# Optimization experiments

Hardware: AMD Instinct MI355X
Metric: run time of the kernel (lower is better)

The kernel has to match this reference:

```python
import jax, jax.numpy as jnp
import numpy as np

B, S, D, H, DK, DFF = 4, 2048, 512, 8, 64, 2048
MAX_DIST = 2047  # effective_dist = min(MAX_DIST, S-1) = S-1, required by the skew reshape
EPS = 1e-6


def setup_inputs() -> dict:
    key = jax.random.key(0)
    ks = jax.random.split(key, 12)
    w = lambda k, shape: jax.random.normal(k, shape, jnp.float32) * 0.02
    return {
        "x": jax.random.normal(ks[0], (B, S, D), jnp.float32),
        "mask": jnp.tril(jnp.ones((1, 1, S, S), jnp.int32)),  # causal
        "wq": w(ks[1], (D, D)),
        "wk": w(ks[2], (D, D)),
        "wv": w(ks[3], (D, D)),
        "w0": w(ks[4], (D, D)),
        "b0": jnp.zeros((D,), jnp.float32),
        "rel_emb": w(ks[5], (H, MAX_DIST + 1, DK)),
        "ln1_g": jnp.ones((D,), jnp.float32),
        "ln1_b": jnp.zeros((D,), jnp.float32),
        "ln2_g": jnp.ones((D,), jnp.float32),
        "ln2_b": jnp.zeros((D,), jnp.float32),
        "ff_w1": w(ks[6], (D, DFF)),
        "ff_b1": jnp.zeros((DFF,), jnp.float32),
        "ff_w2": w(ks[7], (DFF, D)),
        "ff_b2": jnp.zeros((D,), jnp.float32),
    }


def _layernorm(t, g, b):
    mu = t.mean(-1, keepdims=True)
    var = ((t - mu) ** 2).mean(-1, keepdims=True)
    return (t - mu) * jax.lax.rsqrt(var + EPS) * g + b


def _rel_scores(q, rel_emb):
    # q: [B,H,S,DK]; rel_emb: [H, MAX_DIST+1, DK]
    eff = min(MAX_DIST, S - 1)                      # static
    q_er = jnp.einsum('bhid,hrd->bhir', q, rel_emb[:, :eff + 1])  # [B,H,S,S]
    padded = jnp.pad(q_er, ((0, 0), (0, 0), (0, 0), (1, 0)))      # [B,H,S,S+1]
    # skew trick: reinterpret and drop first row -> [B,H,S,S]
    return padded.reshape(B, H, S + 1, S)[:, :, 1:, :]


def reference(x, mask, wq, wk, wv, w0, b0, rel_emb,
              ln1_g, ln1_b, ln2_g, ln2_b, ff_w1, ff_b1, ff_w2, ff_b2):
    scale = float(np.sqrt(DK))
    # --- self-attention sublayer (pre-norm residual) ---
    h = _layernorm(x, ln1_g, ln1_b)
    q = (h @ wq).reshape(B, S, H, DK).transpose(0, 2, 1, 3)  # [B,H,S,DK]
    k = (h @ wk).reshape(B, S, H, DK).transpose(0, 2, 1, 3)
    v = (h @ wv).reshape(B, S, H, DK).transpose(0, 2, 1, 3)
    content = jnp.einsum('bhid,bhjd->bhij', q, k) / scale     # [B,H,S,S]
    scores = content + _rel_scores(q, rel_emb)
    scores = jnp.where(mask == 0, jnp.float32(-1e9), scores)
    probs = jax.nn.softmax(scores, axis=-1)
    attn = jnp.einsum('bhij,bhjd->bhid', probs, v)            # [B,H,S,DK]
    attn = attn.transpose(0, 2, 1, 3).reshape(B, S, D)
    x = x + (attn @ w0 + b0)
    # --- feed-forward sublayer (pre-norm residual) ---
    h2 = _layernorm(x, ln2_g, ln2_b)
    ff = jax.nn.relu(h2 @ ff_w1 + ff_b1) @ ff_w2 + ff_b2
    return x + ff
```

## Files before the change

kernel.cpp:

```cpp
#include <hip/hip_runtime.h>
#include <hip/hip_bf16.h>

#define SB 2048
#define DB 512
#define HB 8
#define DKB 64
#define DFB 2048
#define BATCH 4
#define BSTR 92

typedef __attribute__((ext_vector_type(8))) short bf16x8;
typedef __attribute__((ext_vector_type(4))) float f32x4;
typedef __attribute__((ext_vector_type(2))) float f32x2;
typedef __attribute__((ext_vector_type(2))) unsigned u32x2;
typedef __attribute__((ext_vector_type(4))) short s16x4;

static __device__ __forceinline__ short f2bf(float x) {
  union { float f; unsigned u; } v; v.f = x;
  unsigned r = (v.u + 0x7fffu + ((v.u >> 16) & 1u)) >> 16;
  return (short)(unsigned short)r;
}

static __device__ __forceinline__ float bflo(unsigned u) {
  union { unsigned x; float f; } v; v.x = u << 16; return v.f;
}
static __device__ __forceinline__ float bfhi(unsigned u) {
  union { unsigned x; float f; } v; v.x = u & 0xffff0000u; return v.f;
}

static __device__ __forceinline__ unsigned pack2bf(float a, float b) {
  return (unsigned)(unsigned short)f2bf(a) | ((unsigned)(unsigned short)f2bf(b) << 16);
}

static __device__ __forceinline__ f32x4 mfma16(bf16x8 a, bf16x8 b, f32x4 c) {
  return __builtin_amdgcn_mfma_f32_16x16x32_bf16(a, b, c, 0, 0, 0);
}

static __device__ __forceinline__ float fexp2(float x) {
#if __has_builtin(__builtin_amdgcn_exp2f)
  return __builtin_amdgcn_exp2f(x);
#else
  float r;
  asm("v_exp_f32 %0, %1" : "=v"(r) : "v"(x));
  return r;
#endif
}

static __device__ __forceinline__ void gload_lds16(const short* g, short* l) {
  __builtin_amdgcn_global_load_lds(
      (const __attribute__((address_space(1))) unsigned*)g,
      (__attribute__((address_space(3))) unsigned*)l, 16, 0, 0);
}

__global__ __launch_bounds__(256) void conv_kernel(const float* __restrict__ src,
                                                   short* __restrict__ dst, int n) {
  int i = blockIdx.x * 256 + threadIdx.x;
  if (i < n) dst[i] = f2bf(src[i]);
}

__global__ __launch_bounds__(256) void tconv_kernel(const float* __restrict__ src,
                                                    short* __restrict__ dst,
                                                    int K, int N, float scale) {
  __shared__ float t[64][65];
  int n0 = blockIdx.x * 64, k0 = blockIdx.y * 64;
  int cn = threadIdx.x & 63, rk = threadIdx.x >> 6;
#pragma unroll
  for (int r = 0; r < 16; ++r)
    t[rk + r * 4][cn] = src[(size_t)(k0 + rk + r * 4) * N + n0 + cn];
  __syncthreads();
#pragma unroll
  for (int r = 0; r < 16; ++r)
    dst[(size_t)(n0 + rk + r * 4) * K + k0 + cn] = f2bf(t[cn][rk + r * 4] * scale);
}

__global__ __launch_bounds__(256) void tconv4_kernel(
    const float* __restrict__ s0, const float* __restrict__ s1,
    const float* __restrict__ s2, const float* __restrict__ s3,
    short* __restrict__ dst) {
  __shared__ float t[64][65];
  int z = blockIdx.z;
  const float* src = z == 0 ? s0 : (z == 1 ? s1 : (z == 2 ? s2 : s3));
  float scale = (z == 0) ? 1.4426950408889634f : ((z == 1) ? 0.125f : 1.f);
  short* d = dst + (size_t)z * 512 * 512;
  int n0 = blockIdx.x * 64, k0 = blockIdx.y * 64;
  int cn = threadIdx.x & 63, rk = threadIdx.x >> 6;
#pragma unroll
  for (int r = 0; r < 16; ++r)
    t[rk + r * 4][cn] = src[(size_t)(k0 + rk + r * 4) * 512 + n0 + cn];
  __syncthreads();
#pragma unroll
  for (int r = 0; r < 16; ++r)
    d[(size_t)(n0 + rk + r * 4) * 512 + k0 + cn] = f2bf(t[cn][rk + r * 4] * scale);
}

__global__ __launch_bounds__(256) void ln_kernel(const float* __restrict__ in,
                                                 const float* __restrict__ g,
                                                 const float* __restrict__ bb,
                                                 short* __restrict__ out) {
  int w = threadIdx.x >> 6, l = threadIdx.x & 63;
  size_t row = (size_t)blockIdx.x * 4 + w;
  const float* xr = in + row * DB;
  f32x4 v0 = *(const f32x4*)(xr + l * 8);
  f32x4 v1 = *(const f32x4*)(xr + l * 8 + 4);
  float s = (v0[0] + v0[1]) + (v0[2] + v0[3]) + (v1[0] + v1[1]) + (v1[2] + v1[3]);
  float s2 = (v0[0] * v0[0] + v0[1] * v0[1]) + (v0[2] * v0[2] + v0[3] * v0[3]) +
             (v1[0] * v1[0] + v1[1] * v1[1]) + (v1[2] * v1[2] + v1[3] * v1[3]);
#pragma unroll
  for (int off = 1; off < 64; off <<= 1) {
    s += __shfl_xor(s, off, 64);
    s2 += __shfl_xor(s2, off, 64);
  }
  float mean = s * (1.f / DB);
  float var = s2 * (1.f / DB) - mean * mean;
  float rstd = rsqrtf(var + 1e-6f);
  f32x4 g0 = *(const f32x4*)(g + l * 8);
  f32x4 g1 = *(const f32x4*)(g + l * 8 + 4);
  f32x4 b0 = *(const f32x4*)(bb + l * 8);
  f32x4 b1 = *(const f32x4*)(bb + l * 8 + 4);
  bf16x8 ov;
#pragma unroll
  for (int e = 0; e < 4; ++e) ov[e] = f2bf((v0[e] - mean) * rstd * g0[e] + b0[e]);
#pragma unroll
  for (int e = 0; e < 4; ++e) ov[4 + e] = f2bf((v1[e] - mean) * rstd * g1[e] + b1[e]);
  *(bf16x8*)(out + row * DB + l * 8) = ov;
}

template <int KD, int EPI>
__global__ __launch_bounds__(256) void gemm_kernel(
    const short* __restrict__ A, const short* __restrict__ BT,
    const float* __restrict__ bias, const float* __restrict__ resid,
    short* __restrict__ o0, short* __restrict__ o1, short* __restrict__ o2,
    float* __restrict__ of) {
  __shared__ short As[2][8192];
  __shared__ short Bs[2][8192];
  int tid = threadIdx.x;
  int l = tid & 63, w = tid >> 6;
  int wr = w >> 1, wc = w & 1;
  int lr = l & 15, lq = l >> 4;
  int row0 = blockIdx.y * 128;
  int col0 = blockIdx.x * 128;

  f32x4 acc[4][4];
#pragma unroll
  for (int a = 0; a < 4; ++a)
#pragma unroll
    for (int b = 0; b < 4; ++b) acc[a][b] = (f32x4){0.f, 0.f, 0.f, 0.f};

  int srow = tid >> 3;
  int scol = (tid & 7) ^ (srow & 7);
  const short* gA = A + (size_t)(row0 + srow) * KD + scol * 8;
  const short* gB = BT + (size_t)(col0 + srow) * KD + scol * 8;

  auto stage = [&](int buf, int k0) {
#pragma unroll
    for (int ro = 0; ro < 4; ++ro) {
      gload_lds16(gA + (size_t)(ro * 32) * KD + k0, As[buf] + ro * 2048 + w * 512);
      gload_lds16(gB + (size_t)(ro * 32) * KD + k0, Bs[buf] + ro * 2048 + w * 512);
    }
  };

  stage(0, 0);
  __syncthreads();
  int cur = 0;
  for (int k0 = 0; k0 < KD; k0 += 64) {
    if (k0 + 64 < KD) stage(cur ^ 1, k0 + 64);
#pragma unroll
    for (int kk = 0; kk < 2; ++kk) {
      bf16x8 af[4], bfv[4];
#pragma unroll
      for (int a = 0; a < 4; ++a) {
        int rk = wr * 64 + a * 16 + lr;
        af[a] = *(const bf16x8*)(As[cur] + rk * 64 + ((((kk << 2) | lq) ^ (rk & 7)) << 3));
      }
#pragma unroll
      for (int b = 0; b < 4; ++b) {
        int rk = wc * 64 + b * 16 + lr;
        bfv[b] = *(const bf16x8*)(Bs[cur] + rk * 64 + ((((kk << 2) | lq) ^ (rk & 7)) << 3));
      }
#pragma unroll
      for (int a = 0; a < 4; ++a)
#pragma unroll
        for (int b = 0; b < 4; ++b)
          acc[a][b] = mfma16(af[a], bfv[b], acc[a][b]);
    }
    __syncthreads();
    cur ^= 1;
  }

#pragma unroll
  for (int a = 0; a < 4; ++a)
#pragma unroll
    for (int b = 0; b < 4; ++b) {
      size_t colb = (size_t)col0 + wc * 64 + b * 16 + lr;
      if (EPI == 0 && (int)(colb >> 9) == 2) {
        int d = (int)(colb & 63);
        size_t rowb = (size_t)row0 + wr * 64 + a * 16 + lq * 4;
        size_t b_ = rowb >> 11, s_ = rowb & 2047;
        size_t bh = b_ * HB + (int)((colb >> 6) & 7);
        s16x4 pkv;
#pragma unroll
        for (int r = 0; r < 4; ++r) pkv[r] = f2bf(acc[a][b][r]);
        *(s16x4*)(o2 + (bh * DKB + d) * SB + s_) = pkv;
        continue;
      }
#pragma unroll
      for (int r = 0; r < 4; ++r) {
        size_t row = (size_t)row0 + wr * 64 + a * 16 + lq * 4 + r;
        size_t col = colb;
        float val = acc[a][b][r];
        if (EPI == 0) {
          int sect = (int)(col >> 9);
          int hh = (int)((col >> 6) & 7);
          int d = (int)(col & 63);
          size_t b_ = row >> 11, s_ = row & 2047;
          size_t bh = b_ * HB + hh;
          short bv = f2bf(val);
          if (sect == 0) o0[(bh * SB + s_) * DKB + d] = bv;
          else o1[(bh * SB + s_) * DKB + d] = bv;
        } else if (EPI == 1) {
          of[row * DB + col] = resid[row * DB + col] + val + bias[col];
        } else {
          float tv = val + bias[col];
          o0[row * DFB + col] = f2bf(tv > 0.f ? tv : 0.f);
        }
      }
    }
}

template <int KD>
__global__ __launch_bounds__(256) void gemm64_kernel(
    const short* __restrict__ A, const short* __restrict__ BT,
    const float* __restrict__ bias, const float* __restrict__ resid,
    float* __restrict__ of) {
  __shared__ short As[2][8192];
  __shared__ short Bs[2][4096];
  int tid = threadIdx.x;
  int l = tid & 63, w = tid >> 6;
  int lr = l & 15, lq = l >> 4;
  int row0 = blockIdx.y * 128;
  int col0 = blockIdx.x * 64;

  f32x4 acc[2][4];
#pragma unroll
  for (int a = 0; a < 2; ++a)
#pragma unroll
    for (int b = 0; b < 4; ++b) acc[a][b] = (f32x4){0.f, 0.f, 0.f, 0.f};

  int srow = tid >> 3;
  int scol = (tid & 7) ^ (srow & 7);
  const short* gA = A + (size_t)(row0 + srow) * KD + scol * 8;
  const short* gB = BT + (size_t)(col0 + srow) * KD + scol * 8;

  auto stage = [&](int buf, int k0) {
#pragma unroll
    for (int ro = 0; ro < 4; ++ro)
      gload_lds16(gA + (size_t)(ro * 32) * KD + k0, As[buf] + ro * 2048 + w * 512);
#pragma unroll
    for (int ro = 0; ro < 2; ++ro)
      gload_lds16(gB + (size_t)(ro * 32) * KD + k0, Bs[buf] + ro * 2048 + w * 512);
  };

  stage(0, 0);
  __syncthreads();
  int cur = 0;
  for (int k0 = 0; k0 < KD; k0 += 64) {
    if (k0 + 64 < KD) stage(cur ^ 1, k0 + 64);
#pragma unroll
    for (int kk = 0; kk < 2; ++kk) {
      bf16x8 af[2], bfv[4];
#pragma unroll
      for (int a = 0; a < 2; ++a) {
        int rk = w * 32 + a * 16 + lr;
        af[a] = *(const bf16x8*)(As[cur] + rk * 64 + ((((kk << 2) | lq) ^ (rk & 7)) << 3));
      }
#pragma unroll
      for (int b = 0; b < 4; ++b) {
        int rk = b * 16 + lr;
        bfv[b] = *(const bf16x8*)(Bs[cur] + rk * 64 + ((((kk << 2) | lq) ^ (rk & 7)) << 3));
      }
#pragma unroll
      for (int a = 0; a < 2; ++a)
#pragma unroll
        for (int b = 0; b < 4; ++b)
          acc[a][b] = mfma16(af[a], bfv[b], acc[a][b]);
    }
    __syncthreads();
    cur ^= 1;
  }

#pragma unroll
  for (int a = 0; a < 2; ++a)
#pragma unroll
    for (int b = 0; b < 4; ++b)
#pragma unroll
      for (int r = 0; r < 4; ++r) {
        size_t row = (size_t)row0 + w * 32 + a * 16 + lq * 4 + r;
        size_t col = (size_t)col0 + b * 16 + lr;
        of[row * DB + col] = resid[row * DB + col] + acc[a][b][r] + bias[col];
      }
}

static __device__ __forceinline__ void e_phase_lds(const short* Ebuf, int w, int ph,
                                                   bf16x8 q0, bf16x8 q1,
                                                   short* bdx, int lr, int lq) {
  bf16x8 ef[10];
#pragma unroll
  for (int nt = 0; nt < 5; ++nt) {
    int re = 48 - 16 * w + nt * 16 + lr;
    int sr = (re + ph) & 127;
    const short* eb = Ebuf + sr * 64;
    ef[nt * 2] = *(const bf16x8*)(eb + ((lq ^ (sr & 7)) << 3));
    ef[nt * 2 + 1] = *(const bf16x8*)(eb + (((lq + 4) ^ (sr & 7)) << 3));
  }
  const f32x4 zz = {0.f, 0.f, 0.f, 0.f};
#pragma unroll
  for (int nt = 0; nt < 5; ++nt) {
    f32x4 rr = mfma16(ef[nt * 2 + 1], q1, mfma16(ef[nt * 2], q0, zz));
    u32x2 pk = {pack2bf(rr[0], rr[1]), pack2bf(rr[2], rr[3])};
    *(u32x2*)((char*)bdx + lr * (BSTR * 2) + (nt * 16 + lq * 4) * 2) = pk;
  }
}

static __device__ __forceinline__ void sm_step(const f32x4* sc, const short* bd,
                                               short* pb, f32x4* acc,
                                               float& mrun, float& lsum,
                                               int i0, int j0, int lr, int lq) {
  int bbase = lq * 4 + 15 - lr;
  int o = bbase & 3;
  unsigned shb = (unsigned)(o & 1) * 16;
  bool hi2 = (o >= 2);
  float bv[4][4];
#pragma unroll
  for (int hh = 0; hh < 4; ++hh) {
    int w0 = (hh * 16 + bbase) & ~3;
    const unsigned* p = (const unsigned*)(bd + lr * BSTR + w0);
    unsigned W0 = p[0], W1 = p[1], W2 = p[2], W3 = p[3];
    unsigned X0 = hi2 ? W1 : W0;
    unsigned X1 = hi2 ? W2 : W1;
    unsigned X2 = hi2 ? W3 : W2;
    unsigned out0 = (unsigned)((((unsigned long long)X1 << 32) | X0) >> shb);
    unsigned out1 = (unsigned)((((unsigned long long)X2 << 32) | X1) >> shb);
    bv[hh][0] = bflo(out0);
    bv[hh][1] = bfhi(out0);
    bv[hh][2] = bflo(out1);
    bv[hh][3] = bfhi(out1);
  }
  float s[4][4];
  if (j0 + 63 > i0) {
    int thr = i0 + lr - j0;
#pragma unroll
    for (int hh = 0; hh < 4; ++hh)
#pragma unroll
      for (int r = 0; r < 4; ++r) {
        int n = hh * 16 + lq * 4 + r;
        float v = sc[hh][r] + bv[hh][r];
        s[hh][r] = (n <= thr) ? v : -1e30f;
      }
  } else {
#pragma unroll
    for (int hh = 0; hh < 4; ++hh)
#pragma unroll
      for (int r = 0; r < 4; ++r) s[hh][r] = sc[hh][r] + bv[hh][r];
  }
  float m0 = fmaxf(fmaxf(s[0][0], s[0][1]), fmaxf(s[0][2], s[0][3]));
  float m1 = fmaxf(fmaxf(s[1][0], s[1][1]), fmaxf(s[1][2], s[1][3]));
  float m2 = fmaxf(fmaxf(s[2][0], s[2][1]), fmaxf(s[2][2], s[2][3]));
  float m3 = fmaxf(fmaxf(s[3][0], s[3][1]), fmaxf(s[3][2], s[3][3]));
  float tm = fmaxf(fmaxf(m0, m1), fmaxf(m2, m3));
  if (!__all(tm <= mrun + 8.f)) {
    float tr = fmaxf(tm, __shfl_xor(tm, 16, 64));
    tr = fmaxf(tr, __shfl_xor(tr, 32, 64));
    float mnew = fmaxf(mrun, tr);
    float corr = fexp2(mrun - mnew);
    mrun = mnew;
    lsum *= corr;
#pragma unroll
    for (int dt = 0; dt < 4; ++dt) acc[dt] *= corr;
  }
#pragma unroll
  for (int hh = 0; hh < 4; ++hh) {
    float p0 = fexp2(s[hh][0] - mrun);
    float p1 = fexp2(s[hh][1] - mrun);
    float p2 = fexp2(s[hh][2] - mrun);
    float p3 = fexp2(s[hh][3] - mrun);
    lsum += (p0 + p1) + (p2 + p3);
    u32x2 pk = {pack2bf(p0, p1), pack2bf(p2, p3)};
    int byteoff = lr * (BSTR * 2) + ((((hh << 1) | (lq >> 1)) ^ (lr & 7)) << 4) + ((lq & 1) << 3);
    *(u32x2*)((char*)pb + byteoff) = pk;
  }
}

static __device__ __forceinline__ void pv_step(const short* pb, const bf16x8* vf,
                                               f32x4* acc, int lr, int lq) {
#pragma unroll
  for (int kc = 0; kc < 2; ++kc) {
    bf16x8 pf = *(const bf16x8*)((const char*)pb + lr * (BSTR * 2) +
                                 ((((kc << 2) | lq) ^ (lr & 7)) << 4));
    __builtin_amdgcn_s_setprio(1);
#pragma unroll
    for (int dt = 0; dt < 4; ++dt)
      acc[dt] = mfma16(vf[kc * 4 + dt], pf, acc[dt]);
    __builtin_amdgcn_s_setprio(0);
  }
}

static __device__ __forceinline__ void attn_out(const f32x4* acc, float lsum,
                                                short* out, int bh, int i0,
                                                int lr, int lq) {
  float lt = lsum + __shfl_xor(lsum, 16, 64);
  lt += __shfl_xor(lt, 32, 64);
  float inv = 1.f / lt;
  int b_ = bh >> 3, hd = bh & 7;
  short* orow = out + ((size_t)(b_ * SB + i0 + lr) * DB + hd * 64);
#pragma unroll
  for (int dt = 0; dt < 4; ++dt) {
    s16x4 pkv;
#pragma unroll
    for (int r = 0; r < 4; ++r) pkv[r] = f2bf(acc[dt][r] * inv);
    *(s16x4*)(orow + dt * 16 + lq * 4) = pkv;
  }
}

__global__ __launch_bounds__(256, 2) void attn_kernel(
    const short* __restrict__ Q, const short* __restrict__ Kb,
    const short* __restrict__ VT, const short* __restrict__ Eb,
    short* __restrict__ out) {
  __shared__ short Ks[4096];
  __shared__ short Vs[4096];
  __shared__ short Elo_s[8192];
  __shared__ short Ehi_s[8192];
  __shared__ short bandP[4][2][16][BSTR];
  int tid = threadIdx.x;
  int l = tid & 63, w = tid >> 6;
  int lr = l & 15, lq = l >> 4;
  int bid = blockIdx.x;
  int s = bid >> 3;
  int bh = (bid & 7) * 4 + (s >> 4);
  int g = s & 15;
  int qb0 = g << 6;
  int qb1 = (31 - g) << 6;
  int i0lo = qb0 + (w << 4);
  int i0hi = qb1 + (w << 4);
  const short* Qh = Q + (size_t)bh * SB * DKB;
  const short* Kh = Kb + (size_t)bh * SB * DKB;
  const short* Vh = VT + (size_t)bh * DKB * SB;
  const short* Eh = Eb + (size_t)(bh & 7) * SB * DKB;

  bf16x8 ql0 = *(const bf16x8*)(Qh + (size_t)(i0lo + lr) * DKB + lq * 8);
  bf16x8 ql1 = *(const bf16x8*)(Qh + (size_t)(i0lo + lr) * DKB + 32 + lq * 8);
  bf16x8 qh0 = *(const bf16x8*)(Qh + (size_t)(i0hi + lr) * DKB + lq * 8);
  bf16x8 qh1 = *(const bf16x8*)(Qh + (size_t)(i0hi + lr) * DKB + 32 + lq * 8);

  int lrow = l >> 3, lch = l & 7;
  int rKV = (w << 4) + lrow;
  int cKV = lch ^ (rKV & 7);
  int cE = lch ^ lrow;

  const f32x4 zz = {0.f, 0.f, 0.f, 0.f};
  f32x4 accL[4], accH[4];
#pragma unroll
  for (int dt = 0; dt < 4; ++dt) { accL[dt] = zz; accH[dt] = zz; }
  float mL = -1e30f, lsL = 0.f, mH = -1e30f, lsH = 0.f;
  short* bdL = &bandP[w][0][0][0];
  short* bdH = &bandP[w][1][0][0];

  for (int j0 = 0; j0 < qb1 + 64; j0 += 64) {
    gload_lds16(Kh + (size_t)(j0 + rKV) * DKB + cKV * 8, Ks + (w << 10));
    gload_lds16(Kh + (size_t)(j0 + rKV + 8) * DKB + cKV * 8, Ks + (w << 10) + 512);
    gload_lds16(Vh + (size_t)rKV * SB + j0 + cKV * 8, Vs + (w << 10));
    gload_lds16(Vh + (size_t)(rKV + 8) * SB + j0 + cKV * 8, Vs + (w << 10) + 512);
    int rbHi = SB - 64 - qb1 + j0;
    int phHi = rbHi & 64;
    if (j0 == 0) {
#pragma unroll
      for (int ii = 0; ii < 4; ++ii) {
        int rr = (w << 5) + lrow + ii * 8;
        int er = rbHi + rr;
        er = er < SB ? er : SB - 1;
        int slot0 = ((w << 5) + ii * 8 + phHi) & 127;
        gload_lds16(Eh + (size_t)er * DKB + cE * 8, Ehi_s + (slot0 << 6));
      }
    } else {
#pragma unroll
      for (int ii = 0; ii < 2; ++ii) {
        int rr = (w << 4) + lrow + ii * 8;
        int er = rbHi + 64 + rr;
        er = er < SB ? er : SB - 1;
        int slot0 = ((w << 4) + ii * 8 + (phHi ^ 64)) & 127;
        gload_lds16(Eh + (size_t)er * DKB + cE * 8, Ehi_s + (slot0 << 6));
      }
    }
    int rbLo = SB - 64 - qb0 + j0;
    int phLo = rbLo & 64;
    if (j0 <= qb0 + 63) {
      if (j0 == 0) {
#pragma unroll
        for (int ii = 0; ii < 4; ++ii) {
          int rr = (w << 5) + lrow + ii * 8;
          int er = rbLo + rr;
          er = er < SB ? er : SB - 1;
          int slot0 = ((w << 5) + ii * 8 + phLo) & 127;
          gload_lds16(Eh + (size_t)er * DKB + cE * 8, Elo_s + (slot0 << 6));
        }
      } else {
#pragma unroll
        for (int ii = 0; ii < 2; ++ii) {
          int rr = (w << 4) + lrow + ii * 8;
          int er = rbLo + 64 + rr;
          er = er < SB ? er : SB - 1;
          int slot0 = ((w << 4) + ii * 8 + (phLo ^ 64)) & 127;
          gload_lds16(Eh + (size_t)er * DKB + cE * 8, Elo_s + (slot0 << 6));
        }
      }
    }
    __syncthreads();
    bool actLo = (j0 <= i0lo + 15);
    {
      bf16x8 kf[8];
#pragma unroll
      for (int hh = 0; hh < 4; ++hh) {
        int rk = hh * 16 + lr;
        const short* kb = Ks + rk * 64;
        kf[hh * 2] = *(const bf16x8*)(kb + ((lq ^ (rk & 7)) << 3));
        kf[hh * 2 + 1] = *(const bf16x8*)(kb + (((lq + 4) ^ (rk & 7)) << 3));
      }
      f32x4 scH[4], scL[4];
#pragma unroll
      for (int hh = 0; hh < 4; ++hh)
        scH[hh] = mfma16(kf[hh * 2 + 1], qh1, mfma16(kf[hh * 2], qh0, zz));
      if (actLo) {
#pragma unroll
        for (int hh = 0; hh < 4; ++hh)
          scL[hh] = mfma16(kf[hh * 2 + 1], ql1, mfma16(kf[hh * 2], ql0, zz));
      }
      bf16x8 vf[8];
#pragma unroll
      for (int kc = 0; kc < 2; ++kc)
#pragma unroll
        for (int dt = 0; dt < 4; ++dt) {
          int rv = dt * 16 + lr;
          vf[kc * 4 + dt] = *(const bf16x8*)(Vs + rv * 64 +
                                             (((kc * 4 + lq) ^ (rv & 7)) << 3));
        }
      e_phase_lds(Ehi_s, w, phHi, qh0, qh1, bdH, lr, lq);
      if (actLo) e_phase_lds(Elo_s, w, phLo, ql0, ql1, bdL, lr, lq);
      sm_step(scH, bdH, bdH, accH, mH, lsH, i0hi, j0, lr, lq);
      if (actLo) sm_step(scL, bdL, bdL, accL, mL, lsL, i0lo, j0, lr, lq);
      pv_step(bdH, vf, accH, lr, lq);
      if (actLo) pv_step(bdL, vf, accL, lr, lq);
    }
    __syncthreads();
  }
  attn_out(accH, lsH, out, bh, i0hi, lr, lq);
  attn_out(accL, lsL, out, bh, i0lo, lr, lq);
}

extern "C" void kernel_launch(void* const* d_in, const int* in_sizes, int n_in,
                              void* d_out, int out_size, void* d_ws, size_t ws_size,
                              hipStream_t stream) {
  const float* x    = (const float*)d_in[0];
  const float* wq   = (const float*)d_in[2];
  const float* wk   = (const float*)d_in[3];
  const float* wv   = (const float*)d_in[4];
  const float* w0   = (const float*)d_in[5];
  const float* b0   = (const float*)d_in[6];
  const float* rel  = (const float*)d_in[7];
  const float* ln1g = (const float*)d_in[8];
  const float* ln1b = (const float*)d_in[9];
  const float* ln2g = (const float*)d_in[10];
  const float* ln2b = (const float*)d_in[11];
  const float* fw1  = (const float*)d_in[12];
  const float* fb1  = (const float*)d_in[13];
  const float* fw2  = (const float*)d_in[14];
  const float* fb2  = (const float*)d_in[15];
  float* outp = (float*)d_out;

  char* ws = (char*)d_ws;
  size_t off = 0;
  auto alloc = [&](size_t bytes) {
    char* p = ws + off;
    off += (bytes + 255) & ~(size_t)255;
    return p;
  };
  short* wqkvT = (short*)alloc((size_t)1536 * 512 * 2);
  short* w0T   = (short*)alloc((size_t)512 * 512 * 2);
  short* fw1T  = (short*)alloc((size_t)2048 * 512 * 2);
  short* fw2T  = (short*)alloc((size_t)512 * 2048 * 2);
  short* relb  = (short*)alloc((size_t)8 * 2048 * 64 * 2);
  short* hbuf  = (short*)alloc((size_t)8192 * 512 * 2);
  short* Qb    = (short*)alloc((size_t)8192 * 512 * 2);
  short* Kbf   = (short*)alloc((size_t)8192 * 512 * 2);
  short* VTb   = (short*)alloc((size_t)8192 * 512 * 2);
  short* attnb = (short*)alloc((size_t)8192 * 512 * 2);
  float* x2    = (float*)alloc((size_t)8192 * 512 * 4);
  short* ff1 = hbuf;
  short* h2  = attnb;
  (void)w0T;

  dim3 blk(256);
  conv_kernel<<<(8 * 2048 * 64 + 255) / 256, blk, 0, stream>>>(rel, relb, 8 * 2048 * 64);
  tconv4_kernel<<<dim3(8, 8, 4), blk, 0, stream>>>(wq, wk, wv, w0, wqkvT);
  tconv_kernel<<<dim3(32, 8), blk, 0, stream>>>(fw1, fw1T, 512, 2048, 1.f);
  tconv_kernel<<<dim3(8, 32), blk, 0, stream>>>(fw2, fw2T, 2048, 512, 1.f);

  ln_kernel<<<2048, blk, 0, stream>>>(x, ln1g, ln1b, hbuf);
  gemm_kernel<512, 0><<<dim3(12, 64), blk, 0, stream>>>(hbuf, wqkvT, nullptr, nullptr,
                                                        Qb, Kbf, VTb, nullptr);
  attn_kernel<<<512, blk, 0, stream>>>(Qb, Kbf, VTb, relb, attnb);
  gemm64_kernel<512><<<dim3(8, 64), blk, 0, stream>>>(attnb, wqkvT + (size_t)3 * 512 * 512,
                                                      b0, x, x2);
  ln_kernel<<<2048, blk, 0, stream>>>(x2, ln2g, ln2b, h2);
  gemm_kernel<512, 2><<<dim3(16, 64), blk, 0, stream>>>(h2, fw1T, fb1, nullptr,
                                                        ff1, nullptr, nullptr, nullptr);
  gemm64_kernel<2048><<<dim3(8, 64), blk, 0, stream>>>(ff1, fw2T, fb2, x2, outp);
}
```

Baseline: 225.1 us.

## Register-prefetch next K/V/E tiles to overlap global loads with compute

Replaces the direct global-to-LDS loads at the top of each attention iteration with a prologue load followed by register prefetch of the next tile's K, V and relative-embedding rows, issued before the current tile's MFMA work. After compute, the prefetched registers are written into LDS between two barriers. This is meant to hide global memory latency behind the score and PV math, at the cost of more VGPRs (possibly lower occupancy) and an extra barrier per iteration.

```diff
diff --git a/kernel.cpp b/kernel.cpp
--- a/kernel.cpp
+++ b/kernel.cpp
@@ -13,6 +13,7 @@
 typedef __attribute__((ext_vector_type(4))) float f32x4;
 typedef __attribute__((ext_vector_type(2))) float f32x2;
 typedef __attribute__((ext_vector_type(2))) unsigned u32x2;
+typedef __attribute__((ext_vector_type(4))) unsigned u32x4;
 typedef __attribute__((ext_vector_type(4))) short s16x4;
 
 static __device__ __forceinline__ short f2bf(float x) {
@@ -464,57 +465,62 @@
   short* bdL = &bandP[w][0][0][0];
   short* bdH = &bandP[w][1][0][0];
 
-  for (int j0 = 0; j0 < qb1 + 64; j0 += 64) {
-    gload_lds16(Kh + (size_t)(j0 + rKV) * DKB + cKV * 8, Ks + (w << 10));
-    gload_lds16(Kh + (size_t)(j0 + rKV + 8) * DKB + cKV * 8, Ks + (w << 10) + 512);
-    gload_lds16(Vh + (size_t)rKV * SB + j0 + cKV * 8, Vs + (w << 10));
-    gload_lds16(Vh + (size_t)(rKV + 8) * SB + j0 + cKV * 8, Vs + (w << 10) + 512);
-    int rbHi = SB - 64 - qb1 + j0;
-    int phHi = rbHi & 64;
-    if (j0 == 0) {
-#pragma unroll
-      for (int ii = 0; ii < 4; ++ii) {
-        int rr = (w << 5) + lrow + ii * 8;
-        int er = rbHi + rr;
-        er = er < SB ? er : SB - 1;
-        int slot0 = ((w << 5) + ii * 8 + phHi) & 127;
-        gload_lds16(Eh + (size_t)er * DKB + cE * 8, Ehi_s + (slot0 << 6));
-      }
-    } else {
-#pragma unroll
-      for (int ii = 0; ii < 2; ++ii) {
-        int rr = (w << 4) + lrow + ii * 8;
-        int er = rbHi + 64 + rr;
-        er = er < SB ? er : SB - 1;
-        int slot0 = ((w << 4) + ii * 8 + (phHi ^ 64)) & 127;
-        gload_lds16(Eh + (size_t)er * DKB + cE * 8, Ehi_s + (slot0 << 6));
-      }
-    }
-    int rbLo = SB - 64 - qb0 + j0;
-    int phLo = rbLo & 64;
-    if (j0 <= qb0 + 63) {
-      if (j0 == 0) {
-#pragma unroll
-        for (int ii = 0; ii < 4; ++ii) {
-          int rr = (w << 5) + lrow + ii * 8;
-          int er = rbLo + rr;
-          er = er < SB ? er : SB - 1;
-          int slot0 = ((w << 5) + ii * 8 + phLo) & 127;
-          gload_lds16(Eh + (size_t)er * DKB + cE * 8, Elo_s + (slot0 << 6));
-        }
-      } else {
-#pragma unroll
-        for (int ii = 0; ii < 2; ++ii) {
-          int rr = (w << 4) + lrow + ii * 8;
-          int er = rbLo + 64 + rr;
-          er = er < SB ? er : SB - 1;
-          int slot0 = ((w << 4) + ii * 8 + (phLo ^ 64)) & 127;
-          gload_lds16(Eh + (size_t)er * DKB + cE * 8, Elo_s + (slot0 << 6));
-        }
-      }
-    }
-    __syncthreads();
-    bool actLo = (j0 <= i0lo + 15);
+  int ntrips = (qb1 >> 6) + 1;
+
+  {
+    gload_lds16(Kh + (size_t)rKV * DKB + cKV * 8, Ks + (w << 10));
+    gload_lds16(Kh + (size_t)(rKV + 8) * DKB + cKV * 8, Ks + (w << 10) + 512);
+    gload_lds16(Vh + (size_t)rKV * SB + cKV * 8, Vs + (w << 10));
+    gload_lds16(Vh + (size_t)(rKV + 8) * SB + cKV * 8, Vs + (w << 10) + 512);
+    int rbHi0 = SB - 64 - qb1;
+    int phHi0 = rbHi0 & 64;
+#pragma unroll
+    for (int ii = 0; ii < 4; ++ii) {
+      int er = rbHi0 + (w << 5) + lrow + ii * 8;
+      er = er < SB ? er : SB - 1;
+      int slot0 = ((w << 5) + ii * 8 + phHi0) & 127;
+      gload_lds16(Eh + (size_t)er * DKB + cE * 8, Ehi_s + (slot0 << 6));
+    }
+    int rbLo0 = SB - 64 - qb0;
+    int phLo0 = rbLo0 & 64;
+#pragma unroll
+    for (int ii = 0; ii < 4; ++ii) {
+      int er = rbLo0 + (w << 5) + lrow + ii * 8;
+      er = er < SB ? er : SB - 1;
+      int slot0 = ((w << 5) + ii * 8 + phLo0) & 127;
+      gload_lds16(Eh + (size_t)er * DKB + cE * 8, Elo_s + (slot0 << 6));
+    }
+  }
+  __syncthreads();
+
+  u32x4 rK0, rK1, rV0, rV1, rEh0, rEh1, rEl0, rEl1;
+
+  for (int t = 0; t < ntrips; ++t) {
+    int j0 = t << 6;
+    int phHi = (SB - 64 - qb1 + j0) & 64;
+    int phLo = (SB - 64 - qb0 + j0) & 64;
+    bool pf = (t + 1 < ntrips);
+    bool pfLo = (t + 1 <= g);
+    if (pf) {
+      int j0n = j0 + 64;
+      rK0 = *(const u32x4*)(Kh + (size_t)(j0n + rKV) * DKB + cKV * 8);
+      rK1 = *(const u32x4*)(Kh + (size_t)(j0n + rKV + 8) * DKB + cKV * 8);
+      rV0 = *(const u32x4*)(Vh + (size_t)rKV * SB + j0n + cKV * 8);
+      rV1 = *(const u32x4*)(Vh + (size_t)(rKV + 8) * SB + j0n + cKV * 8);
+      int eb0 = SB - 64 - qb1 + j0 + 128 + (w << 4) + lrow;
+      int e0 = eb0 < SB ? eb0 : SB - 1;
+      int e1 = (eb0 + 8) < SB ? (eb0 + 8) : SB - 1;
+      rEh0 = *(const u32x4*)(Eh + (size_t)e0 * DKB + cE * 8);
+      rEh1 = *(const u32x4*)(Eh + (size_t)e1 * DKB + cE * 8);
+      if (pfLo) {
+        int fb0 = SB - 64 - qb0 + j0 + 128 + (w << 4) + lrow;
+        int f0 = fb0 < SB ? fb0 : SB - 1;
+        int f1 = (fb0 + 8) < SB ? (fb0 + 8) : SB - 1;
+        rEl0 = *(const u32x4*)(Eh + (size_t)f0 * DKB + cE * 8);
+        rEl1 = *(const u32x4*)(Eh + (size_t)f1 * DKB + cE * 8);
+      }
+    }
+    bool actLo = (t <= g);
     {
       bf16x8 kf[8];
 #pragma unroll
@@ -549,7 +555,24 @@
       pv_step(bdH, vf, accH, lr, lq);
       if (actLo) pv_step(bdL, vf, accL, lr, lq);
     }
-    __syncthreads();
+    if (pf) {
+      __syncthreads();
+      *(u32x4*)(Ks + (w << 10) + l * 8) = rK0;
+      *(u32x4*)(Ks + (w << 10) + 512 + l * 8) = rK1;
+      *(u32x4*)(Vs + (w << 10) + l * 8) = rV0;
+      *(u32x4*)(Vs + (w << 10) + 512 + l * 8) = rV1;
+      int s0 = ((w << 4) + phHi) & 127;
+      int s1 = ((w << 4) + 8 + phHi) & 127;
+      *(u32x4*)(Ehi_s + (s0 << 6) + l * 8) = rEh0;
+      *(u32x4*)(Ehi_s + (s1 << 6) + l * 8) = rEh1;
+      if (pfLo) {
+        int s2 = ((w << 4) + phLo) & 127;
+        int s3 = ((w << 4) + 8 + phLo) & 127;
+        *(u32x4*)(Elo_s + (s2 << 6) + l * 8) = rEl0;
+        *(u32x4*)(Elo_s + (s3 << 6) + l * 8) = rEl1;
+      }
+      __syncthreads();
+    }
   }
   attn_out(accH, lsH, out, bh, i0hi, lr, lq);
   attn_out(accL, lsL, out, bh, i0lo, lr, lq);
```

Measured after the change: 223.6 us. About the same (-0.7%).
